# Optimization experiments

Measured on AMD Instinct MI355X. Metric: run time of the kernel, lower is better.

## Reference

```python
import jax, jax.numpy as jnp
import numpy as np


def _coord1d(n):
    # make_coord: grid-center coordinates in (-1, 1)
    return -1.0 + 1.0 / n + (2.0 / n) * jnp.arange(n, dtype=jnp.float32)


def _conv1x1(x, w, b):
    # 1x1 conv == channel matmul. x: [B,C,H,W], w: [O,C], b: [O]
    return jnp.einsum('bchw,oc->bohw', x, w) + b[None, :, None, None]


def setup_inputs() -> dict:
    key = jax.random.key(0)
    ks = jax.random.split(key, 8)
    B, C, h, w = 2, 64, 96, 96
    d = 256
    Cin = (C + 2) * 4 + 2  # 266
    s = lambda k, shp, fan: (jax.random.normal(k, shp, jnp.float32) / np.sqrt(fan)).astype(jnp.float32)
    return {
        'feat': jax.random.normal(ks[0], (B, C, h, w), jnp.float32),
        'w00': s(ks[1], (d, Cin), Cin), 'b00': jnp.zeros((d,), jnp.float32),
        'w1': s(ks[2], (d, d), d), 'b1': jnp.zeros((d,), jnp.float32),
        'w2': s(ks[3], (3, d), d), 'b2': jnp.zeros((3,), jnp.float32),
        'ws1': s(ks[4], (C, C), C), 'bs1': jnp.zeros((C,), jnp.float32),
        'ws2': s(ks[5], (3, C), C), 'bs2': jnp.zeros((3,), jnp.float32),
        'target_h': 384, 'target_w': 384,
    }


def reference(feat, w00, b00, w1, b1, w2, b2, ws1, bs1, ws2, bs2, target_h, target_w):
    B, C, h, w = feat.shape
    H, W = int(target_h), int(target_w)
    # HR query coordinates, shared across batch. cy along height (dim0), cx along width (dim1)
    cy = jnp.broadcast_to(_coord1d(H)[:, None], (H, W))
    cx = jnp.broadcast_to(_coord1d(W)[None, :], (H, W))
    rx = 1.0 / h  # = 2/h/2, half-pixel radius along height
    ry = 1.0 / w
    eps_shift = 1e-6

    def nearest(c, n):
        # grid_sample nearest, align_corners=False: unnormalize then round (half-to-even, as nearbyint)
        u = ((c + 1.0) * n - 1.0) / 2.0
        return jnp.clip(jnp.round(u).astype(jnp.int32), 0, n - 1)

    rel_coords, feat_s, areas = [], [], []
    for vx in (-1.0, 1.0):
        for vy in (-1.0, 1.0):
            sy = jnp.clip(cy + vx * rx + eps_shift, -1.0 + 1e-6, 1.0 - 1e-6)
            sx = jnp.clip(cx + vy * ry + eps_shift, -1.0 + 1e-6, 1.0 - 1e-6)
            iy = nearest(sy, h)  # [H,W]
            ix = nearest(sx, w)
            feat_s.append(feat[:, :, iy, ix])  # [B,C,H,W] gather
            # nearest-sampled LR pixel-center coords (what grid_sample(pos_lr,...) returns)
            old_y = -1.0 + 1.0 / h + (2.0 / h) * iy.astype(jnp.float32)
            old_x = -1.0 + 1.0 / w + (2.0 / w) * ix.astype(jnp.float32)
            rel_y = (cy - old_y) * h
            rel_x = (cx - old_x) * w
            rel_coords.append(jnp.stack([rel_y, rel_x], 0))  # [2,H,W]
            areas.append(jnp.abs(rel_y * rel_x) + 1e-9)

    tot = areas[0] + areas[1] + areas[2] + areas[3]
    # LIIF area swap: 0<->3, 1<->2
    areas = [areas[3], areas[2], areas[1], areas[0]]
    feat_s = [f * (a / tot)[None, None] for f, a in zip(feat_s, areas)]

    scale_h, scale_w = H / h, W / w
    cell_h = (2.0 / H) * max(scale_h / 4.0, 1.0) * h
    cell_w = (2.0 / W) * max(scale_w / 4.0, 1.0) * w
    rel_cell = jnp.broadcast_to(
        jnp.array([cell_h, cell_w], jnp.float32)[None, :, None, None], (B, 2, H, W))
    rels = jnp.broadcast_to(jnp.concatenate(rel_coords, 0)[None], (B, 8, H, W))
    grid = jnp.concatenate([rels, *feat_s, rel_cell], axis=1)  # [B,266,H,W]

    x = _conv1x1(grid, w00, b00)
    ret = _conv1x1(jax.nn.gelu(_conv1x1(x, w1, b1), approximate=False), w2, b2)

    # shortcut branch: 1x1 MLP on LR feat, then bilinear border sample at coord
    sc = _conv1x1(jax.nn.relu(_conv1x1(feat, ws1, bs1)), ws2, bs2)  # [B,3,h,w]
    uy = ((cy + 1.0) * h - 1.0) / 2.0
    ux = ((cx + 1.0) * w - 1.0) / 2.0
    y0 = jnp.floor(uy)
    x0 = jnp.floor(ux)
    wy = uy - y0
    wx = ux - x0
    y0i = jnp.clip(y0.astype(jnp.int32), 0, h - 1)
    y1i = jnp.clip(y0.astype(jnp.int32) + 1, 0, h - 1)
    x0i = jnp.clip(x0.astype(jnp.int32), 0, w - 1)
    x1i = jnp.clip(x0.astype(jnp.int32) + 1, 0, w - 1)
    samp = (sc[:, :, y0i, x0i] * ((1 - wy) * (1 - wx))[None, None]
            + sc[:, :, y0i, x1i] * ((1 - wy) * wx)[None, None]
            + sc[:, :, y1i, x0i] * (wy * (1 - wx))[None, None]
            + sc[:, :, y1i, x1i] * (wy * wx)[None, None])
    return ret + samp
```

## Files before the change

### kernel.cpp

```cpp
#include <hip/hip_runtime.h>

typedef __bf16 bf16x8 __attribute__((ext_vector_type(8)));
typedef __bf16 bf16x4 __attribute__((ext_vector_type(4)));
typedef float f32x4 __attribute__((ext_vector_type(4)));

namespace {
constexpr int Bn = 2, Cn = 64, hn = 96, wn = 96, Hn = 384, Wn = 384;
constexpr int CIN = 266;
constexpr int TM = 64;
constexpr int SP = 296;
constexpr int L1_FRAGS = 9 * 16 * 64;
constexpr int L2_FRAGS = 8 * 16 * 64;
constexpr int L3_FRAGS = 8 * 64;
constexpr int N_FRAGS = L1_FRAGS + L2_FRAGS + L3_FRAGS;
constexpr int SC_OFF_BYTES = N_FRAGS * 16;
constexpr int B1EFF_OFF_BYTES = SC_OFF_BYTES + Bn * 3 * hn * wn * 4;
constexpr int FRAG_BLOCKS = N_FRAGS / 256;
constexpr int SC_BLOCKS = (Bn * hn * wn) / 256;
}

__global__ void prep_all(const float* __restrict__ w00, const float* __restrict__ w1,
                         const float* __restrict__ w2, const float* __restrict__ b00,
                         const float* __restrict__ b1,
                         const float* __restrict__ feat, const float* __restrict__ ws1,
                         const float* __restrict__ bs1, const float* __restrict__ ws2,
                         const float* __restrict__ bs2,
                         __bf16* __restrict__ wb, float* __restrict__ b1eff,
                         float* __restrict__ sc)
{
    const int bid = blockIdx.x;
    if (bid < FRAG_BLOCKS) {
        const int f = bid * 256 + threadIdx.x;
        bf16x8 v;
        if (f < L1_FRAGS) {
            const int k0 = f >> 10;
            const int mb = (f >> 6) & 15;
            const int l  = f & 63;
            const int m  = mb * 16 + (l & 15);
            const int kb = k0 * 32 + (l >> 4) * 8;
#pragma unroll
            for (int j = 0; j < 8; j++)
                v[j] = (kb + j < CIN) ? (__bf16)w00[m * CIN + kb + j] : (__bf16)0.f;
        } else if (f < L1_FRAGS + L2_FRAGS) {
            const int g = f - L1_FRAGS;
            const int k0 = g >> 10;
            const int mb = (g >> 6) & 15;
            const int l  = g & 63;
            const int m  = mb * 16 + (l & 15);
            const int kb = k0 * 32 + (l >> 4) * 8;
#pragma unroll
            for (int j = 0; j < 8; j++) v[j] = (__bf16)w1[m * 256 + kb + j];
        } else {
            const int g = f - (L1_FRAGS + L2_FRAGS);
            const int k0 = g >> 6;
            const int l  = g & 63;
            const int m  = l & 15;
            const int kb = k0 * 32 + (l >> 4) * 8;
#pragma unroll
            for (int j = 0; j < 8; j++)
                v[j] = (m < 3) ? (__bf16)w2[m * 256 + kb + j] : (__bf16)0.f;
        }
        *(bf16x8*)(wb + f * 8) = v;
        return;
    }
    if (bid == FRAG_BLOCKS) {
        __shared__ float cb[256];
        const int o = threadIdx.x;
        cb[o] = b00[o] + 0.5f * (w00[o * CIN + 264] + w00[o * CIN + 265]);
        __syncthreads();
        float v = b1[o];
#pragma unroll 4
        for (int k = 0; k < 256; k++) v = fmaf(w1[o * 256 + k], cb[k], v);
        b1eff[o] = v;
        return;
    }
    const int t = (bid - FRAG_BLOCKS - 1) * 256 + threadIdx.x;
    if (t >= Bn * hn * wn) return;
    const int b = t / (hn * wn);
    const int yx = t % (hn * wn);
    const float* fp = feat + b * Cn * hn * wn + yx;
    float f[Cn];
#pragma unroll
    for (int c = 0; c < Cn; c++) f[c] = fp[c * hn * wn];
    float o0 = bs2[0], o1 = bs2[1], o2 = bs2[2];
#pragma unroll 1
    for (int co = 0; co < Cn; co += 4) {
        float v0 = bs1[co], v1 = bs1[co + 1], v2 = bs1[co + 2], v3 = bs1[co + 3];
        const float* wr = ws1 + co * Cn;
#pragma unroll
        for (int ci = 0; ci < Cn; ci++) {
            const float fv = f[ci];
            v0 = fmaf(wr[ci], fv, v0);
            v1 = fmaf(wr[Cn + ci], fv, v1);
            v2 = fmaf(wr[2 * Cn + ci], fv, v2);
            v3 = fmaf(wr[3 * Cn + ci], fv, v3);
        }
        v0 = fmaxf(v0, 0.f); v1 = fmaxf(v1, 0.f); v2 = fmaxf(v2, 0.f); v3 = fmaxf(v3, 0.f);
#pragma unroll
        for (int u = 0; u < 4; u++) {
            const float vv = (u == 0) ? v0 : (u == 1) ? v1 : (u == 2) ? v2 : v3;
            o0 = fmaf(ws2[co + u], vv, o0);
            o1 = fmaf(ws2[Cn + co + u], vv, o1);
            o2 = fmaf(ws2[2 * Cn + co + u], vv, o2);
        }
    }
    sc[(b * 3 + 0) * hn * wn + yx] = o0;
    sc[(b * 3 + 1) * hn * wn + yx] = o1;
    sc[(b * 3 + 2) * hn * wn + yx] = o2;
}

__device__ __forceinline__ float gelu_fast(float x) {
    const float d0 = -2.302118074f;
    const float d1 = -0.1029453754f;
    float t = x * x;
    float a = x * fmaf(t, d1, d0);
    float e = __builtin_amdgcn_exp2f(a);
    return x * __builtin_amdgcn_rcpf(1.f + e);
}

__device__ __forceinline__ bf16x4 pack4(f32x4 x) {
    bf16x4 v;
    v[0] = (__bf16)x[0]; v[1] = (__bf16)x[1]; v[2] = (__bf16)x[2]; v[3] = (__bf16)x[3];
    return v;
}


#define MF(A, B, C) __builtin_amdgcn_mfma_f32_16x16x32_bf16((A), (B), (C), 0, 0, 0)

#define GSTEP(k0, W0, W1, W2, W3) do {                                          \
    const bf16x8 g0 = *(const bf16x8*)&Abuf[     lane16][(k0) * 32 + quad * 8]; \
    const bf16x8 g1 = *(const bf16x8*)&Abuf[16 + lane16][(k0) * 32 + quad * 8]; \
    const bf16x8 g2 = *(const bf16x8*)&Abuf[32 + lane16][(k0) * 32 + quad * 8]; \
    const bf16x8 g3 = *(const bf16x8*)&Abuf[48 + lane16][(k0) * 32 + quad * 8]; \
    a00 = MF(W0, g0, a00); a01 = MF(W1, g0, a01); a02 = MF(W2, g0, a02); a03 = MF(W3, g0, a03); \
    a10 = MF(W0, g1, a10); a11 = MF(W1, g1, a11); a12 = MF(W2, g1, a12); a13 = MF(W3, g1, a13); \
    a20 = MF(W0, g2, a20); a21 = MF(W1, g2, a21); a22 = MF(W2, g2, a22); a23 = MF(W3, g2, a23); \
    a30 = MF(W0, g3, a30); a31 = MF(W1, g3, a31); a32 = MF(W2, g3, a32); a33 = MF(W3, g3, a33); \
} while (0)

#define LDW(W0, W1, W2, W3, src, kk) do {             \
    W0 = (src)[((kk) * 16 + mb0 + 0) * 64 + lane];    \
    W1 = (src)[((kk) * 16 + mb0 + 1) * 64 + lane];    \
    W2 = (src)[((kk) * 16 + mb0 + 2) * 64 + lane];    \
    W3 = (src)[((kk) * 16 + mb0 + 3) * 64 + lane];    \
} while (0)

#define ZACC4(n) a##n##0 = zf; a##n##1 = zf; a##n##2 = zf; a##n##3 = zf

__global__ __launch_bounds__(256, 3) void liif_main(
    const float* __restrict__ feat, const float* __restrict__ b1eff,
    const float* __restrict__ b2v, const __bf16* __restrict__ wb,
    const float* __restrict__ sc, float* __restrict__ out)
{
    __shared__ __align__(16) __bf16 Abuf[TM][SP];

    const int t = threadIdx.x;
    const int wv = t >> 6;
    const int lane = t & 63;
    const int lane16 = lane & 15;
    const int quad = lane >> 4;
    const int mb0 = wv * 4;

    constexpr int NWG = Bn * Hn * (Wn / TM);
    const int lt = (blockIdx.x & 7) * (NWG / 8) + (blockIdx.x >> 3);
    constexpr int TPR = Wn / TM;
    const int tx = lt % TPR;
    const int Y = (lt / TPR) % Hn;
    const int b = lt / (TPR * Hn);
    const int X0 = tx * TM;

    const float cy = -1.f + 1.f / Hn + (2.f / Hn) * (float)Y;

    const bf16x8* wf1 = (const bf16x8*)wb;
    const bf16x8* wf2 = wf1 + L1_FRAGS;
    const bf16x8* w2f = wf1 + (L1_FRAGS + L2_FRAGS);

    bf16x8 wE0, wE1, wE2, wE3, wO0, wO1, wO2, wO3;
    LDW(wE0, wE1, wE2, wE3, wf1, 0);
    LDW(wO0, wO1, wO2, wO3, wf1, 1);

    {
        const int p = lane;
        const int j = wv;
        const int X = X0 + p;
        const float cx = -1.f + 1.f / Wn + (2.f / Wn) * (float)X;
        float rely[4], relx[4], area[4];
        int iyv[4], ixv[4];
#pragma unroll
        for (int c = 0; c < 4; c++) {
            const float vx = (c & 2) ? 1.f : -1.f;
            const float vy = (c & 1) ? 1.f : -1.f;
            float sy = fminf(fmaxf(cy + vx * (1.f / hn) + 1e-6f, -1.f + 1e-6f), 1.f - 1e-6f);
            float sx = fminf(fmaxf(cx + vy * (1.f / wn) + 1e-6f, -1.f + 1e-6f), 1.f - 1e-6f);
            float uy = ((sy + 1.f) * hn - 1.f) * 0.5f;
            float ux = ((sx + 1.f) * wn - 1.f) * 0.5f;
            int iy = min(max((int)rintf(uy), 0), hn - 1);
            int ix = min(max((int)rintf(ux), 0), wn - 1);
            float oy = -1.f + 1.f / hn + (2.f / hn) * (float)iy;
            float ox = -1.f + 1.f / wn + (2.f / wn) * (float)ix;
            rely[c] = (cy - oy) * hn;
            relx[c] = (cx - ox) * wn;
            area[c] = fabsf(rely[c] * relx[c]) + 1e-9f;
            iyv[c] = iy; ixv[c] = ix;
        }
        const float tot = area[0] + area[1] + area[2] + area[3];
        const float wj = area[3 - j] / tot;

        if (j == 0) {
            bf16x8 v;
#pragma unroll
            for (int c = 0; c < 4; c++) { v[2 * c] = (__bf16)rely[c]; v[2 * c + 1] = (__bf16)relx[c]; }
            *(bf16x8*)&Abuf[p][0] = v;
        }
        const float* fb = feat + ((b * Cn) * hn + iyv[j]) * wn + ixv[j];
#pragma unroll
        for (int c8 = 0; c8 < 8; c8++) {
            bf16x8 v;
#pragma unroll
            for (int cc = 0; cc < 8; cc++)
                v[cc] = (__bf16)(fb[(c8 * 8 + cc) * (hn * wn)] * wj);
            *(bf16x8*)&Abuf[p][8 + 64 * j + c8 * 8] = v;
        }
        if (j == 3) {
            bf16x8 z;
#pragma unroll
            for (int cc = 0; cc < 8; cc++) z[cc] = (__bf16)0.f;
            *(bf16x8*)&Abuf[p][264] = z;
            *(bf16x8*)&Abuf[p][272] = z;
            *(bf16x8*)&Abuf[p][280] = z;
        }
    }
    __syncthreads();

    const f32x4 zf = (f32x4){0.f, 0.f, 0.f, 0.f};
    f32x4 a00, a01, a02, a03, a10, a11, a12, a13;
    f32x4 a20, a21, a22, a23, a30, a31, a32, a33;
    ZACC4(0); ZACC4(1); ZACC4(2); ZACC4(3);

    GSTEP(0, wE0, wE1, wE2, wE3); LDW(wE0, wE1, wE2, wE3, wf1, 2);
    GSTEP(1, wO0, wO1, wO2, wO3); LDW(wO0, wO1, wO2, wO3, wf1, 3);
    GSTEP(2, wE0, wE1, wE2, wE3); LDW(wE0, wE1, wE2, wE3, wf1, 4);
    GSTEP(3, wO0, wO1, wO2, wO3); LDW(wO0, wO1, wO2, wO3, wf1, 5);
    GSTEP(4, wE0, wE1, wE2, wE3); LDW(wE0, wE1, wE2, wE3, wf1, 6);
    GSTEP(5, wO0, wO1, wO2, wO3); LDW(wO0, wO1, wO2, wO3, wf1, 7);
    GSTEP(6, wE0, wE1, wE2, wE3); LDW(wE0, wE1, wE2, wE3, wf1, 8);
    GSTEP(7, wO0, wO1, wO2, wO3); LDW(wO0, wO1, wO2, wO3, wf2, 0);
    GSTEP(8, wE0, wE1, wE2, wE3); LDW(wE0, wE1, wE2, wE3, wf2, 1);

    __syncthreads();
    {
        const int ch0 = mb0 * 16 + quad * 4;
        *(bf16x4*)&Abuf[     lane16][ch0     ] = pack4(a00);
        *(bf16x4*)&Abuf[16 + lane16][ch0     ] = pack4(a10);
        *(bf16x4*)&Abuf[32 + lane16][ch0     ] = pack4(a20);
        *(bf16x4*)&Abuf[48 + lane16][ch0     ] = pack4(a30);
        *(bf16x4*)&Abuf[     lane16][ch0 + 16] = pack4(a01);
        *(bf16x4*)&Abuf[16 + lane16][ch0 + 16] = pack4(a11);
        *(bf16x4*)&Abuf[32 + lane16][ch0 + 16] = pack4(a21);
        *(bf16x4*)&Abuf[48 + lane16][ch0 + 16] = pack4(a31);
        *(bf16x4*)&Abuf[     lane16][ch0 + 32] = pack4(a02);
        *(bf16x4*)&Abuf[16 + lane16][ch0 + 32] = pack4(a12);
        *(bf16x4*)&Abuf[32 + lane16][ch0 + 32] = pack4(a22);
        *(bf16x4*)&Abuf[48 + lane16][ch0 + 32] = pack4(a32);
        *(bf16x4*)&Abuf[     lane16][ch0 + 48] = pack4(a03);
        *(bf16x4*)&Abuf[16 + lane16][ch0 + 48] = pack4(a13);
        *(bf16x4*)&Abuf[32 + lane16][ch0 + 48] = pack4(a23);
        *(bf16x4*)&Abuf[48 + lane16][ch0 + 48] = pack4(a33);
    }
    __syncthreads();

    ZACC4(0); ZACC4(1); ZACC4(2); ZACC4(3);

    GSTEP(0, wO0, wO1, wO2, wO3); LDW(wO0, wO1, wO2, wO3, wf2, 2);
    GSTEP(1, wE0, wE1, wE2, wE3); LDW(wE0, wE1, wE2, wE3, wf2, 3);
    GSTEP(2, wO0, wO1, wO2, wO3); LDW(wO0, wO1, wO2, wO3, wf2, 4);
    GSTEP(3, wE0, wE1, wE2, wE3); LDW(wE0, wE1, wE2, wE3, wf2, 5);
    GSTEP(4, wO0, wO1, wO2, wO3); LDW(wO0, wO1, wO2, wO3, wf2, 6);
    GSTEP(5, wE0, wE1, wE2, wE3); LDW(wE0, wE1, wE2, wE3, wf2, 7);
    GSTEP(6, wO0, wO1, wO2, wO3); wO0 = w2f[0 * 64 + lane];
    GSTEP(7, wE0, wE1, wE2, wE3); wE0 = w2f[1 * 64 + lane];

    __syncthreads();
    {
        const int ch0 = mb0 * 16 + quad * 4;
        const f32x4 bi0 = *(const f32x4*)&b1eff[ch0];
        const f32x4 bi1 = *(const f32x4*)&b1eff[ch0 + 16];
        const f32x4 bi2 = *(const f32x4*)&b1eff[ch0 + 32];
        const f32x4 bi3 = *(const f32x4*)&b1eff[ch0 + 48];
#define GEL4(x, bi) { bf16x4 v; v[0] = (__bf16)gelu_fast((x)[0] + (bi)[0]); \
        v[1] = (__bf16)gelu_fast((x)[1] + (bi)[1]); \
        v[2] = (__bf16)gelu_fast((x)[2] + (bi)[2]); \
        v[3] = (__bf16)gelu_fast((x)[3] + (bi)[3]); vv = v; }
        bf16x4 vv;
        GEL4(a00, bi0); *(bf16x4*)&Abuf[     lane16][ch0     ] = vv;
        GEL4(a10, bi0); *(bf16x4*)&Abuf[16 + lane16][ch0     ] = vv;
        GEL4(a20, bi0); *(bf16x4*)&Abuf[32 + lane16][ch0     ] = vv;
        GEL4(a30, bi0); *(bf16x4*)&Abuf[48 + lane16][ch0     ] = vv;
        GEL4(a01, bi1); *(bf16x4*)&Abuf[     lane16][ch0 + 16] = vv;
        GEL4(a11, bi1); *(bf16x4*)&Abuf[16 + lane16][ch0 + 16] = vv;
        GEL4(a21, bi1); *(bf16x4*)&Abuf[32 + lane16][ch0 + 16] = vv;
        GEL4(a31, bi1); *(bf16x4*)&Abuf[48 + lane16][ch0 + 16] = vv;
        GEL4(a02, bi2); *(bf16x4*)&Abuf[     lane16][ch0 + 32] = vv;
        GEL4(a12, bi2); *(bf16x4*)&Abuf[16 + lane16][ch0 + 32] = vv;
        GEL4(a22, bi2); *(bf16x4*)&Abuf[32 + lane16][ch0 + 32] = vv;
        GEL4(a32, bi2); *(bf16x4*)&Abuf[48 + lane16][ch0 + 32] = vv;
        GEL4(a03, bi3); *(bf16x4*)&Abuf[     lane16][ch0 + 48] = vv;
        GEL4(a13, bi3); *(bf16x4*)&Abuf[16 + lane16][ch0 + 48] = vv;
        GEL4(a23, bi3); *(bf16x4*)&Abuf[32 + lane16][ch0 + 48] = vv;
        GEL4(a33, bi3); *(bf16x4*)&Abuf[48 + lane16][ch0 + 48] = vv;
#undef GEL4
    }
    __syncthreads();

    f32x4 acc3 = zf;
#define YF(k0) (*(const bf16x8*)&Abuf[wv * 16 + lane16][(k0) * 32 + quad * 8])
    acc3 = MF(wO0, YF(0), acc3); wO0 = w2f[2 * 64 + lane];
    acc3 = MF(wE0, YF(1), acc3); wE0 = w2f[3 * 64 + lane];
    acc3 = MF(wO0, YF(2), acc3); wO0 = w2f[4 * 64 + lane];
    acc3 = MF(wE0, YF(3), acc3); wE0 = w2f[5 * 64 + lane];
    acc3 = MF(wO0, YF(4), acc3); wO0 = w2f[6 * 64 + lane];
    acc3 = MF(wE0, YF(5), acc3); wE0 = w2f[7 * 64 + lane];
    acc3 = MF(wO0, YF(6), acc3);
    acc3 = MF(wE0, YF(7), acc3);
#undef YF

    if (quad == 0) {
        const int pix = wv * 16 + lane16;
        const int X = X0 + pix;
        const float uy = ((cy + 1.f) * hn - 1.f) * 0.5f;
        const float fy = floorf(uy);
        const float wy = uy - fy;
        const int y0i = min(max((int)fy, 0), hn - 1);
        const int y1i = min(max((int)fy + 1, 0), hn - 1);
        const float cx = -1.f + 1.f / Wn + (2.f / Wn) * (float)X;
        const float ux = ((cx + 1.f) * wn - 1.f) * 0.5f;
        const float fx = floorf(ux);
        const float wx = ux - fx;
        const int x0i = min(max((int)fx, 0), wn - 1);
        const int x1i = min(max((int)fx + 1, 0), wn - 1);
        const float w00b = (1.f - wy) * (1.f - wx), w01b = (1.f - wy) * wx;
        const float w10b = wy * (1.f - wx), w11b = wy * wx;
#pragma unroll
        for (int r = 0; r < 3; r++) {
            const float* scb = sc + (b * 3 + r) * (hn * wn);
            const float samp = scb[y0i * wn + x0i] * w00b + scb[y0i * wn + x1i] * w01b
                             + scb[y1i * wn + x0i] * w10b + scb[y1i * wn + x1i] * w11b;
            out[((b * 3 + r) * Hn + Y) * Wn + X] = acc3[r] + b2v[r] + samp;
        }
    }
}

extern "C" void kernel_launch(void* const* d_in, const int* in_sizes, int n_in,
                              void* d_out, int out_size, void* d_ws, size_t ws_size,
                              hipStream_t stream)
{
    const float* feat = (const float*)d_in[0];
    const float* w00  = (const float*)d_in[1];
    const float* b00  = (const float*)d_in[2];
    const float* w1   = (const float*)d_in[3];
    const float* b1   = (const float*)d_in[4];
    const float* w2   = (const float*)d_in[5];
    const float* b2   = (const float*)d_in[6];
    const float* ws1  = (const float*)d_in[7];
    const float* bs1  = (const float*)d_in[8];
    const float* ws2  = (const float*)d_in[9];
    const float* bs2  = (const float*)d_in[10];
    float* out = (float*)d_out;

    __bf16* wb    = (__bf16*)d_ws;
    float* scbuf  = (float*)((char*)d_ws + SC_OFF_BYTES);
    float* b1eff  = (float*)((char*)d_ws + B1EFF_OFF_BYTES);

    prep_all<<<FRAG_BLOCKS + 1 + SC_BLOCKS, 256, 0, stream>>>(
        w00, w1, w2, b00, b1, feat, ws1, bs1, ws2, bs2, wb, b1eff, scbuf);
    liif_main<<<Bn * Hn * (Wn / TM), 256, 0, stream>>>(feat, b1eff, b2, wb, scbuf, out);
}
```

Before: 198.7 us.

## Switch main GEMMs to 32x32x16 MFMA and gather from channel-last feat

Replaces the 16x16x32 MFMA tiling of the two 256-wide layers with 32x32x16 bf16 MFMAs, with each wave owning 64 output channels across two 32-pixel row blocks. The weight fragments are re-laid out to match, and the number of weight fragments held in registers drops. The prep kernel also writes a channel-last copy of feat so the nearest-neighbour gather in the main kernel uses contiguous float4 loads instead of channel-strided scalar loads. The cost is an extra feat transpose write and larger accumulator register tiles.

Result: slower. 215.3 us (+8.4%).

```diff
diff --git a/kernel.cpp b/kernel.cpp
--- a/kernel.cpp
+++ b/kernel.cpp
@@ -3,18 +3,22 @@
 typedef __bf16 bf16x8 __attribute__((ext_vector_type(8)));
 typedef __bf16 bf16x4 __attribute__((ext_vector_type(4)));
 typedef float f32x4 __attribute__((ext_vector_type(4)));
+typedef float f32x16 __attribute__((ext_vector_type(16)));
 
 namespace {
 constexpr int Bn = 2, Cn = 64, hn = 96, wn = 96, Hn = 384, Wn = 384;
 constexpr int CIN = 266;
 constexpr int TM = 64;
 constexpr int SP = 296;
-constexpr int L1_FRAGS = 9 * 16 * 64;
-constexpr int L2_FRAGS = 8 * 16 * 64;
+constexpr int L1_KS = 18;
+constexpr int L2_KS = 16;
+constexpr int L1_FRAGS = L1_KS * 8 * 64;
+constexpr int L2_FRAGS = L2_KS * 8 * 64;
 constexpr int L3_FRAGS = 8 * 64;
 constexpr int N_FRAGS = L1_FRAGS + L2_FRAGS + L3_FRAGS;
 constexpr int SC_OFF_BYTES = N_FRAGS * 16;
 constexpr int B1EFF_OFF_BYTES = SC_OFF_BYTES + Bn * 3 * hn * wn * 4;
+constexpr int FEATT_OFF_BYTES = B1EFF_OFF_BYTES + 1024;
 constexpr int FRAG_BLOCKS = N_FRAGS / 256;
 constexpr int SC_BLOCKS = (Bn * hn * wn) / 256;
 }
@@ -26,28 +30,30 @@
                          const float* __restrict__ bs1, const float* __restrict__ ws2,
                          const float* __restrict__ bs2,
                          __bf16* __restrict__ wb, float* __restrict__ b1eff,
-                         float* __restrict__ sc)
+                         float* __restrict__ sc, float* __restrict__ featT)
 {
     const int bid = blockIdx.x;
     if (bid < FRAG_BLOCKS) {
         const int f = bid * 256 + threadIdx.x;
         bf16x8 v;
         if (f < L1_FRAGS) {
-            const int k0 = f >> 10;
-            const int mb = (f >> 6) & 15;
+            const int fr = f >> 6;
             const int l  = f & 63;
-            const int m  = mb * 16 + (l & 15);
-            const int kb = k0 * 32 + (l >> 4) * 8;
+            const int ks = fr >> 3;
+            const int mb = fr & 7;
+            const int m  = mb * 32 + (l & 31);
+            const int kb = ks * 16 + (l >> 5) * 8;
 #pragma unroll
             for (int j = 0; j < 8; j++)
                 v[j] = (kb + j < CIN) ? (__bf16)w00[m * CIN + kb + j] : (__bf16)0.f;
         } else if (f < L1_FRAGS + L2_FRAGS) {
             const int g = f - L1_FRAGS;
-            const int k0 = g >> 10;
-            const int mb = (g >> 6) & 15;
+            const int fr = g >> 6;
             const int l  = g & 63;
-            const int m  = mb * 16 + (l & 15);
-            const int kb = k0 * 32 + (l >> 4) * 8;
+            const int ks = fr >> 3;
+            const int mb = fr & 7;
+            const int m  = mb * 32 + (l & 31);
+            const int kb = ks * 16 + (l >> 5) * 8;
 #pragma unroll
             for (int j = 0; j < 8; j++) v[j] = (__bf16)w1[m * 256 + kb + j];
         } else {
@@ -82,6 +88,13 @@
     float f[Cn];
 #pragma unroll
     for (int c = 0; c < Cn; c++) f[c] = fp[c * hn * wn];
+    {
+        float* ft = featT + t * Cn;
+#pragma unroll
+        for (int c4 = 0; c4 < Cn / 4; c4++)
+            *(f32x4*)&ft[c4 * 4] =
+                (f32x4){f[4 * c4], f[4 * c4 + 1], f[4 * c4 + 2], f[4 * c4 + 3]};
+    }
     float o0 = bs2[0], o1 = bs2[1], o2 = bs2[2];
 #pragma unroll 1
     for (int co = 0; co < Cn; co += 4) {
@@ -125,30 +138,25 @@
 }
 
 
-#define MF(A, B, C) __builtin_amdgcn_mfma_f32_16x16x32_bf16((A), (B), (C), 0, 0, 0)
-
-#define GSTEP(k0, W0, W1, W2, W3) do {                                          \
-    const bf16x8 g0 = *(const bf16x8*)&Abuf[     lane16][(k0) * 32 + quad * 8]; \
-    const bf16x8 g1 = *(const bf16x8*)&Abuf[16 + lane16][(k0) * 32 + quad * 8]; \
-    const bf16x8 g2 = *(const bf16x8*)&Abuf[32 + lane16][(k0) * 32 + quad * 8]; \
-    const bf16x8 g3 = *(const bf16x8*)&Abuf[48 + lane16][(k0) * 32 + quad * 8]; \
-    a00 = MF(W0, g0, a00); a01 = MF(W1, g0, a01); a02 = MF(W2, g0, a02); a03 = MF(W3, g0, a03); \
-    a10 = MF(W0, g1, a10); a11 = MF(W1, g1, a11); a12 = MF(W2, g1, a12); a13 = MF(W3, g1, a13); \
-    a20 = MF(W0, g2, a20); a21 = MF(W1, g2, a21); a22 = MF(W2, g2, a22); a23 = MF(W3, g2, a23); \
-    a30 = MF(W0, g3, a30); a31 = MF(W1, g3, a31); a32 = MF(W2, g3, a32); a33 = MF(W3, g3, a33); \
+#define MF16(A, B, C) __builtin_amdgcn_mfma_f32_16x16x32_bf16((A), (B), (C), 0, 0, 0)
+#define MF32(A, B, C) __builtin_amdgcn_mfma_f32_32x32x16_bf16((A), (B), (C), 0, 0, 0)
+
+#define G32(ks, W0, W1) do {                                                    \
+    const bf16x8 g0 = *(const bf16x8*)&Abuf[     l31][(ks) * 16 + hh * 8];      \
+    const bf16x8 g1 = *(const bf16x8*)&Abuf[32 + l31][(ks) * 16 + hh * 8];      \
+    c00 = MF32(W0, g0, c00); c01 = MF32(W0, g1, c01);                           \
+    c10 = MF32(W1, g0, c10); c11 = MF32(W1, g1, c11);                           \
 } while (0)
 
-#define LDW(W0, W1, W2, W3, src, kk) do {             \
-    W0 = (src)[((kk) * 16 + mb0 + 0) * 64 + lane];    \
-    W1 = (src)[((kk) * 16 + mb0 + 1) * 64 + lane];    \
-    W2 = (src)[((kk) * 16 + mb0 + 2) * 64 + lane];    \
-    W3 = (src)[((kk) * 16 + mb0 + 3) * 64 + lane];    \
+#define LDW2(W0, W1, src, kk) do {                    \
+    W0 = (src)[((kk) * 8 + mbp + 0) * 64 + lane];     \
+    W1 = (src)[((kk) * 8 + mbp + 1) * 64 + lane];     \
 } while (0)
 
-#define ZACC4(n) a##n##0 = zf; a##n##1 = zf; a##n##2 = zf; a##n##3 = zf
+#define PKS(v, g) pack4((f32x4){(v)[4 * (g)], (v)[4 * (g) + 1], (v)[4 * (g) + 2], (v)[4 * (g) + 3]})
 
 __global__ __launch_bounds__(256, 3) void liif_main(
-    const float* __restrict__ feat, const float* __restrict__ b1eff,
+    const float* __restrict__ featT, const float* __restrict__ b1eff,
     const float* __restrict__ b2v, const __bf16* __restrict__ wb,
     const float* __restrict__ sc, float* __restrict__ out)
 {
@@ -159,7 +167,9 @@
     const int lane = t & 63;
     const int lane16 = lane & 15;
     const int quad = lane >> 4;
-    const int mb0 = wv * 4;
+    const int l31 = lane & 31;
+    const int hh = lane >> 5;
+    const int mbp = wv * 2;
 
     constexpr int NWG = Bn * Hn * (Wn / TM);
     const int lt = (blockIdx.x & 7) * (NWG / 8) + (blockIdx.x >> 3);
@@ -175,9 +185,9 @@
     const bf16x8* wf2 = wf1 + L1_FRAGS;
     const bf16x8* w2f = wf1 + (L1_FRAGS + L2_FRAGS);
 
-    bf16x8 wE0, wE1, wE2, wE3, wO0, wO1, wO2, wO3;
-    LDW(wE0, wE1, wE2, wE3, wf1, 0);
-    LDW(wO0, wO1, wO2, wO3, wf1, 1);
+    bf16x8 wE0, wE1, wO0, wO1;
+    LDW2(wE0, wE1, wf1, 0);
+    LDW2(wO0, wO1, wf1, 1);
 
     {
         const int p = lane;
@@ -212,13 +222,16 @@
             for (int c = 0; c < 4; c++) { v[2 * c] = (__bf16)rely[c]; v[2 * c + 1] = (__bf16)relx[c]; }
             *(bf16x8*)&Abuf[p][0] = v;
         }
-        const float* fb = feat + ((b * Cn) * hn + iyv[j]) * wn + ixv[j];
+        const float* fb = featT + ((b * hn + iyv[j]) * wn + ixv[j]) * Cn;
 #pragma unroll
         for (int c8 = 0; c8 < 8; c8++) {
+            const f32x4 u0 = *(const f32x4*)&fb[c8 * 8];
+            const f32x4 u1 = *(const f32x4*)&fb[c8 * 8 + 4];
             bf16x8 v;
-#pragma unroll
-            for (int cc = 0; cc < 8; cc++)
-                v[cc] = (__bf16)(fb[(c8 * 8 + cc) * (hn * wn)] * wj);
+            v[0] = (__bf16)(u0[0] * wj); v[1] = (__bf16)(u0[1] * wj);
+            v[2] = (__bf16)(u0[2] * wj); v[3] = (__bf16)(u0[3] * wj);
+            v[4] = (__bf16)(u1[0] * wj); v[5] = (__bf16)(u1[1] * wj);
+            v[6] = (__bf16)(u1[2] * wj); v[7] = (__bf16)(u1[3] * wj);
             *(bf16x8*)&Abuf[p][8 + 64 * j + c8 * 8] = v;
         }
         if (j == 3) {
@@ -232,96 +245,121 @@
     }
     __syncthreads();
 
-    const f32x4 zf = (f32x4){0.f, 0.f, 0.f, 0.f};
-    f32x4 a00, a01, a02, a03, a10, a11, a12, a13;
-    f32x4 a20, a21, a22, a23, a30, a31, a32, a33;
-    ZACC4(0); ZACC4(1); ZACC4(2); ZACC4(3);
-
-    GSTEP(0, wE0, wE1, wE2, wE3); LDW(wE0, wE1, wE2, wE3, wf1, 2);
-    GSTEP(1, wO0, wO1, wO2, wO3); LDW(wO0, wO1, wO2, wO3, wf1, 3);
-    GSTEP(2, wE0, wE1, wE2, wE3); LDW(wE0, wE1, wE2, wE3, wf1, 4);
-    GSTEP(3, wO0, wO1, wO2, wO3); LDW(wO0, wO1, wO2, wO3, wf1, 5);
-    GSTEP(4, wE0, wE1, wE2, wE3); LDW(wE0, wE1, wE2, wE3, wf1, 6);
-    GSTEP(5, wO0, wO1, wO2, wO3); LDW(wO0, wO1, wO2, wO3, wf1, 7);
-    GSTEP(6, wE0, wE1, wE2, wE3); LDW(wE0, wE1, wE2, wE3, wf1, 8);
-    GSTEP(7, wO0, wO1, wO2, wO3); LDW(wO0, wO1, wO2, wO3, wf2, 0);
-    GSTEP(8, wE0, wE1, wE2, wE3); LDW(wE0, wE1, wE2, wE3, wf2, 1);
+    const f32x16 zf = {0.f, 0.f, 0.f, 0.f, 0.f, 0.f, 0.f, 0.f,
+                       0.f, 0.f, 0.f, 0.f, 0.f, 0.f, 0.f, 0.f};
+    f32x16 c00 = zf, c01 = zf, c10 = zf, c11 = zf;
+
+    G32(0,  wE0, wE1); LDW2(wE0, wE1, wf1, 2);
+    G32(1,  wO0, wO1); LDW2(wO0, wO1, wf1, 3);
+    G32(2,  wE0, wE1); LDW2(wE0, wE1, wf1, 4);
+    G32(3,  wO0, wO1); LDW2(wO0, wO1, wf1, 5);
+    G32(4,  wE0, wE1); LDW2(wE0, wE1, wf1, 6);
+    G32(5,  wO0, wO1); LDW2(wO0, wO1, wf1, 7);
+    G32(6,  wE0, wE1); LDW2(wE0, wE1, wf1, 8);
+    G32(7,  wO0, wO1); LDW2(wO0, wO1, wf1, 9);
+    G32(8,  wE0, wE1); LDW2(wE0, wE1, wf1, 10);
+    G32(9,  wO0, wO1); LDW2(wO0, wO1, wf1, 11);
+    G32(10, wE0, wE1); LDW2(wE0, wE1, wf1, 12);
+    G32(11, wO0, wO1); LDW2(wO0, wO1, wf1, 13);
+    G32(12, wE0, wE1); LDW2(wE0, wE1, wf1, 14);
+    G32(13, wO0, wO1); LDW2(wO0, wO1, wf1, 15);
+    G32(14, wE0, wE1); LDW2(wE0, wE1, wf1, 16);
+    G32(15, wO0, wO1); LDW2(wO0, wO1, wf1, 17);
+    G32(16, wE0, wE1); LDW2(wE0, wE1, wf2, 0);
+    G32(17, wO0, wO1); LDW2(wO0, wO1, wf2, 1);
 
     __syncthreads();
     {
-        const int ch0 = mb0 * 16 + quad * 4;
-        *(bf16x4*)&Abuf[     lane16][ch0     ] = pack4(a00);
-        *(bf16x4*)&Abuf[16 + lane16][ch0     ] = pack4(a10);
-        *(bf16x4*)&Abuf[32 + lane16][ch0     ] = pack4(a20);
-        *(bf16x4*)&Abuf[48 + lane16][ch0     ] = pack4(a30);
-        *(bf16x4*)&Abuf[     lane16][ch0 + 16] = pack4(a01);
-        *(bf16x4*)&Abuf[16 + lane16][ch0 + 16] = pack4(a11);
-        *(bf16x4*)&Abuf[32 + lane16][ch0 + 16] = pack4(a21);
-        *(bf16x4*)&Abuf[48 + lane16][ch0 + 16] = pack4(a31);
-        *(bf16x4*)&Abuf[     lane16][ch0 + 32] = pack4(a02);
-        *(bf16x4*)&Abuf[16 + lane16][ch0 + 32] = pack4(a12);
-        *(bf16x4*)&Abuf[32 + lane16][ch0 + 32] = pack4(a22);
-        *(bf16x4*)&Abuf[48 + lane16][ch0 + 32] = pack4(a32);
-        *(bf16x4*)&Abuf[     lane16][ch0 + 48] = pack4(a03);
-        *(bf16x4*)&Abuf[16 + lane16][ch0 + 48] = pack4(a13);
-        *(bf16x4*)&Abuf[32 + lane16][ch0 + 48] = pack4(a23);
-        *(bf16x4*)&Abuf[48 + lane16][ch0 + 48] = pack4(a33);
+        const int colA = wv * 64 + hh * 4;
+        const int rA = l31;
+        *(bf16x4*)&Abuf[rA     ][colA +  0] = PKS(c00, 0);
+        *(bf16x4*)&Abuf[rA     ][colA +  8] = PKS(c00, 1);
+        *(bf16x4*)&Abuf[rA     ][colA + 16] = PKS(c00, 2);
+        *(bf16x4*)&Abuf[rA     ][colA + 24] = PKS(c00, 3);
+        *(bf16x4*)&Abuf[rA + 32][colA +  0] = PKS(c01, 0);
+        *(bf16x4*)&Abuf[rA + 32][colA +  8] = PKS(c01, 1);
+        *(bf16x4*)&Abuf[rA + 32][colA + 16] = PKS(c01, 2);
+        *(bf16x4*)&Abuf[rA + 32][colA + 24] = PKS(c01, 3);
+        *(bf16x4*)&Abuf[rA     ][colA + 32] = PKS(c10, 0);
+        *(bf16x4*)&Abuf[rA     ][colA + 40] = PKS(c10, 1);
+        *(bf16x4*)&Abuf[rA     ][colA + 48] = PKS(c10, 2);
+        *(bf16x4*)&Abuf[rA     ][colA + 56] = PKS(c10, 3);
+        *(bf16x4*)&Abuf[rA + 32][colA + 32] = PKS(c11, 0);
+        *(bf16x4*)&Abuf[rA + 32][colA + 40] = PKS(c11, 1);
+        *(bf16x4*)&Abuf[rA + 32][colA + 48] = PKS(c11, 2);
+        *(bf16x4*)&Abuf[rA + 32][colA + 56] = PKS(c11, 3);
     }
     __syncthreads();
 
-    ZACC4(0); ZACC4(1); ZACC4(2); ZACC4(3);
-
-    GSTEP(0, wO0, wO1, wO2, wO3); LDW(wO0, wO1, wO2, wO3, wf2, 2);
-    GSTEP(1, wE0, wE1, wE2, wE3); LDW(wE0, wE1, wE2, wE3, wf2, 3);
-    GSTEP(2, wO0, wO1, wO2, wO3); LDW(wO0, wO1, wO2, wO3, wf2, 4);
-    GSTEP(3, wE0, wE1, wE2, wE3); LDW(wE0, wE1, wE2, wE3, wf2, 5);
-    GSTEP(4, wO0, wO1, wO2, wO3); LDW(wO0, wO1, wO2, wO3, wf2, 6);
-    GSTEP(5, wE0, wE1, wE2, wE3); LDW(wE0, wE1, wE2, wE3, wf2, 7);
-    GSTEP(6, wO0, wO1, wO2, wO3); wO0 = w2f[0 * 64 + lane];
-    GSTEP(7, wE0, wE1, wE2, wE3); wE0 = w2f[1 * 64 + lane];
+    c00 = zf; c01 = zf; c10 = zf; c11 = zf;
+
+    G32(0,  wE0, wE1); LDW2(wE0, wE1, wf2, 2);
+    G32(1,  wO0, wO1); LDW2(wO0, wO1, wf2, 3);
+    G32(2,  wE0, wE1); LDW2(wE0, wE1, wf2, 4);
+    G32(3,  wO0, wO1); LDW2(wO0, wO1, wf2, 5);
+    G32(4,  wE0, wE1); LDW2(wE0, wE1, wf2, 6);
+    G32(5,  wO0, wO1); LDW2(wO0, wO1, wf2, 7);
+    G32(6,  wE0, wE1); LDW2(wE0, wE1, wf2, 8);
+    G32(7,  wO0, wO1); LDW2(wO0, wO1, wf2, 9);
+    G32(8,  wE0, wE1); LDW2(wE0, wE1, wf2, 10);
+    G32(9,  wO0, wO1); LDW2(wO0, wO1, wf2, 11);
+    G32(10, wE0, wE1); LDW2(wE0, wE1, wf2, 12);
+    G32(11, wO0, wO1); LDW2(wO0, wO1, wf2, 13);
+    G32(12, wE0, wE1); LDW2(wE0, wE1, wf2, 14);
+    G32(13, wO0, wO1); LDW2(wO0, wO1, wf2, 15);
+    G32(14, wE0, wE1); wE0 = w2f[0 * 64 + lane];
+    G32(15, wO0, wO1); wE1 = w2f[1 * 64 + lane];
 
     __syncthreads();
     {
-        const int ch0 = mb0 * 16 + quad * 4;
-        const f32x4 bi0 = *(const f32x4*)&b1eff[ch0];
-        const f32x4 bi1 = *(const f32x4*)&b1eff[ch0 + 16];
-        const f32x4 bi2 = *(const f32x4*)&b1eff[ch0 + 32];
-        const f32x4 bi3 = *(const f32x4*)&b1eff[ch0 + 48];
-#define GEL4(x, bi) { bf16x4 v; v[0] = (__bf16)gelu_fast((x)[0] + (bi)[0]); \
-        v[1] = (__bf16)gelu_fast((x)[1] + (bi)[1]); \
-        v[2] = (__bf16)gelu_fast((x)[2] + (bi)[2]); \
-        v[3] = (__bf16)gelu_fast((x)[3] + (bi)[3]); vv = v; }
+        const int colA = wv * 64 + hh * 4;
+        const int rA = l31;
         bf16x4 vv;
-        GEL4(a00, bi0); *(bf16x4*)&Abuf[     lane16][ch0     ] = vv;
-        GEL4(a10, bi0); *(bf16x4*)&Abuf[16 + lane16][ch0     ] = vv;
-        GEL4(a20, bi0); *(bf16x4*)&Abuf[32 + lane16][ch0     ] = vv;
-        GEL4(a30, bi0); *(bf16x4*)&Abuf[48 + lane16][ch0     ] = vv;
-        GEL4(a01, bi1); *(bf16x4*)&Abuf[     lane16][ch0 + 16] = vv;
-        GEL4(a11, bi1); *(bf16x4*)&Abuf[16 + lane16][ch0 + 16] = vv;
-        GEL4(a21, bi1); *(bf16x4*)&Abuf[32 + lane16][ch0 + 16] = vv;
-        GEL4(a31, bi1); *(bf16x4*)&Abuf[48 + lane16][ch0 + 16] = vv;
-        GEL4(a02, bi2); *(bf16x4*)&Abuf[     lane16][ch0 + 32] = vv;
-        GEL4(a12, bi2); *(bf16x4*)&Abuf[16 + lane16][ch0 + 32] = vv;
-        GEL4(a22, bi2); *(bf16x4*)&Abuf[32 + lane16][ch0 + 32] = vv;
-        GEL4(a32, bi2); *(bf16x4*)&Abuf[48 + lane16][ch0 + 32] = vv;
-        GEL4(a03, bi3); *(bf16x4*)&Abuf[     lane16][ch0 + 48] = vv;
-        GEL4(a13, bi3); *(bf16x4*)&Abuf[16 + lane16][ch0 + 48] = vv;
-        GEL4(a23, bi3); *(bf16x4*)&Abuf[32 + lane16][ch0 + 48] = vv;
-        GEL4(a33, bi3); *(bf16x4*)&Abuf[48 + lane16][ch0 + 48] = vv;
-#undef GEL4
+        f32x4 bi;
+#define GEL4S(v, g, bi) { bf16x4 w_; \
+        w_[0] = (__bf16)gelu_fast((v)[4 * (g) + 0] + (bi)[0]); \
+        w_[1] = (__bf16)gelu_fast((v)[4 * (g) + 1] + (bi)[1]); \
+        w_[2] = (__bf16)gelu_fast((v)[4 * (g) + 2] + (bi)[2]); \
+        w_[3] = (__bf16)gelu_fast((v)[4 * (g) + 3] + (bi)[3]); vv = w_; }
+        bi = *(const f32x4*)&b1eff[colA + 0];
+        GEL4S(c00, 0, bi); *(bf16x4*)&Abuf[rA     ][colA +  0] = vv;
+        GEL4S(c01, 0, bi); *(bf16x4*)&Abuf[rA + 32][colA +  0] = vv;
+        bi = *(const f32x4*)&b1eff[colA + 8];
+        GEL4S(c00, 1, bi); *(bf16x4*)&Abuf[rA     ][colA +  8] = vv;
+        GEL4S(c01, 1, bi); *(bf16x4*)&Abuf[rA + 32][colA +  8] = vv;
+        bi = *(const f32x4*)&b1eff[colA + 16];
+        GEL4S(c00, 2, bi); *(bf16x4*)&Abuf[rA     ][colA + 16] = vv;
+        GEL4S(c01, 2, bi); *(bf16x4*)&Abuf[rA + 32][colA + 16] = vv;
+        bi = *(const f32x4*)&b1eff[colA + 24];
+        GEL4S(c00, 3, bi); *(bf16x4*)&Abuf[rA     ][colA + 24] = vv;
+        GEL4S(c01, 3, bi); *(bf16x4*)&Abuf[rA + 32][colA + 24] = vv;
+        bi = *(const f32x4*)&b1eff[colA + 32];
+        GEL4S(c10, 0, bi); *(bf16x4*)&Abuf[rA     ][colA + 32] = vv;
+        GEL4S(c11, 0, bi); *(bf16x4*)&Abuf[rA + 32][colA + 32] = vv;
+        bi = *(const f32x4*)&b1eff[colA + 40];
+        GEL4S(c10, 1, bi); *(bf16x4*)&Abuf[rA     ][colA + 40] = vv;
+        GEL4S(c11, 1, bi); *(bf16x4*)&Abuf[rA + 32][colA + 40] = vv;
+        bi = *(const f32x4*)&b1eff[colA + 48];
+        GEL4S(c10, 2, bi); *(bf16x4*)&Abuf[rA     ][colA + 48] = vv;
+        GEL4S(c11, 2, bi); *(bf16x4*)&Abuf[rA + 32][colA + 48] = vv;
+        bi = *(const f32x4*)&b1eff[colA + 56];
+        GEL4S(c10, 3, bi); *(bf16x4*)&Abuf[rA     ][colA + 56] = vv;
+        GEL4S(c11, 3, bi); *(bf16x4*)&Abuf[rA + 32][colA + 56] = vv;
+#undef GEL4S
     }
     __syncthreads();
 
-    f32x4 acc3 = zf;
+    const f32x4 zf4 = (f32x4){0.f, 0.f, 0.f, 0.f};
+    f32x4 acc3 = zf4;
 #define YF(k0) (*(const bf16x8*)&Abuf[wv * 16 + lane16][(k0) * 32 + quad * 8])
-    acc3 = MF(wO0, YF(0), acc3); wO0 = w2f[2 * 64 + lane];
-    acc3 = MF(wE0, YF(1), acc3); wE0 = w2f[3 * 64 + lane];
-    acc3 = MF(wO0, YF(2), acc3); wO0 = w2f[4 * 64 + lane];
-    acc3 = MF(wE0, YF(3), acc3); wE0 = w2f[5 * 64 + lane];
-    acc3 = MF(wO0, YF(4), acc3); wO0 = w2f[6 * 64 + lane];
-    acc3 = MF(wE0, YF(5), acc3); wE0 = w2f[7 * 64 + lane];
-    acc3 = MF(wO0, YF(6), acc3);
-    acc3 = MF(wE0, YF(7), acc3);
+    acc3 = MF16(wE0, YF(0), acc3); wE0 = w2f[2 * 64 + lane];
+    acc3 = MF16(wE1, YF(1), acc3); wE1 = w2f[3 * 64 + lane];
+    acc3 = MF16(wE0, YF(2), acc3); wE0 = w2f[4 * 64 + lane];
+    acc3 = MF16(wE1, YF(3), acc3); wE1 = w2f[5 * 64 + lane];
+    acc3 = MF16(wE0, YF(4), acc3); wE0 = w2f[6 * 64 + lane];
+    acc3 = MF16(wE1, YF(5), acc3); wE1 = w2f[7 * 64 + lane];
+    acc3 = MF16(wE0, YF(6), acc3);
+    acc3 = MF16(wE1, YF(7), acc3);
 #undef YF
 
     if (quad == 0) {
@@ -370,8 +408,9 @@
     __bf16* wb    = (__bf16*)d_ws;
     float* scbuf  = (float*)((char*)d_ws + SC_OFF_BYTES);
     float* b1eff  = (float*)((char*)d_ws + B1EFF_OFF_BYTES);
+    float* featT  = (float*)((char*)d_ws + FEATT_OFF_BYTES);
 
     prep_all<<<FRAG_BLOCKS + 1 + SC_BLOCKS, 256, 0, stream>>>(
-        w00, w1, w2, b00, b1, feat, ws1, bs1, ws2, bs2, wb, b1eff, scbuf);
-    liif_main<<<Bn * Hn * (Wn / TM), 256, 0, stream>>>(feat, b1eff, b2, wb, scbuf, out);
-}
+        w00, w1, w2, b00, b1, feat, ws1, bs1, ws2, bs2, wb, b1eff, scbuf, featT);
+    liif_main<<<Bn * Hn * (Wn / TM), 256, 0, stream>>>(featT, b1eff, b2, wb, scbuf, out);
+}
```
